# Optimization experiments

Hardware: AMD Instinct MI355X
Metric: run time of the kernel (lower is better)

## Reference

```python
import jax, jax.numpy as jnp
import numpy as np


def setup_inputs() -> dict:
    key = jax.random.key(0)
    k1, k2 = jax.random.split(key)
    B, T, D = 16, 2048, 1024
    inputs = jax.random.normal(k1, (B, T, D), dtype=jnp.float32)
    mask = jax.random.randint(k2, (B, T), 0, 2).astype(bool)
    return {"inputs": inputs, "mask": mask}


def reference(inputs, mask):
    """Batched stream compaction (JIT-compatible ragged representation).

    Original TF layer loops over the batch and, per sample, gathers the
    rows of inputs[i] where mask[i] is True, returning ragged lists of
    (collected_values, valid_indices). Since JAX requires static shapes,
    we return the padded-compacted equivalent:
      collected: [B, T, D]  valid rows moved to the front (order preserved),
                            invalid tail zeroed.
      valid_idx: [B, T]     original timestep index of each collected row,
                            -1 in the padded tail.
      counts:    [B]        number of valid rows per sample, i.e.
                            collected[i, :counts[i]] == ragged segment i.
    """
    # Stable argsort of the inverted mask puts valid positions first,
    # preserving their original order -> single-pass prefix-sum compaction.
    order = jnp.argsort(jnp.logical_not(mask), axis=1, stable=True)      # [B, T]
    sorted_valid = jnp.take_along_axis(mask, order, axis=1)              # [B, T]
    collected = jnp.take_along_axis(inputs, order[:, :, None], axis=1)   # [B, T, D]
    collected = jnp.where(sorted_valid[:, :, None], collected, 0.0)
    valid_idx = jnp.where(sorted_valid, order, -1)
    counts = jnp.sum(mask, axis=1)
    return collected, valid_idx, counts
```

## Files before the change

kernel.cpp:

```cpp
#include <hip/hip_runtime.h>


#define BB 16
#define TT 2048
#define DD 1024
#define ROW4 (DD / 4)

typedef float f4 __attribute__((ext_vector_type(4)));

__global__ __launch_bounds__(256) void scan_kernel(
    const int* __restrict__ mask,
    float* __restrict__ out_vidx,
    float* __restrict__ out_counts,
    int* __restrict__ ws_src,
    int* __restrict__ ws_cnt)
{
    const int b = blockIdx.x;
    const int tid = threadIdx.x;
    const int4* m4 = (const int4*)(mask + b * TT);

    int4 a0 = m4[tid * 2];
    int4 a1 = m4[tid * 2 + 1];
    int vals[8];
    vals[0] = (a0.x != 0); vals[1] = (a0.y != 0);
    vals[2] = (a0.z != 0); vals[3] = (a0.w != 0);
    vals[4] = (a1.x != 0); vals[5] = (a1.y != 0);
    vals[6] = (a1.z != 0); vals[7] = (a1.w != 0);
    int s = 0;
#pragma unroll
    for (int i = 0; i < 8; ++i) s += vals[i];

    __shared__ int sdata[256];
    sdata[tid] = s;
    __syncthreads();
#pragma unroll
    for (int off = 1; off < 256; off <<= 1) {
        int v = (tid >= off) ? sdata[tid - off] : 0;
        __syncthreads();
        sdata[tid] += v;
        __syncthreads();
    }
    const int excl = sdata[tid] - s;
    const int total = sdata[255];

    int pos = excl;
#pragma unroll
    for (int i = 0; i < 8; ++i) {
        if (vals[i]) {
            const int t = tid * 8 + i;
            ws_src[b * TT + pos] = t;
            out_vidx[b * TT + pos] = (float)t;
            ++pos;
        }
    }

    for (int c = total + tid; c < TT; c += 256) {
        out_vidx[b * TT + c] = -1.0f;
    }

    if (tid == 0) {
        ws_cnt[b] = total;
        out_counts[b] = (float)total;
    }
}

__global__ __launch_bounds__(256) void gather_kernel(
    const f4* __restrict__ in,
    const int* __restrict__ ws_src,
    const int* __restrict__ ws_cnt,
    f4* __restrict__ out)
{
    const int tid  = threadIdx.x;
    const int lrow = tid >> 5;
    const int lane = tid & 31;
    const int row  = blockIdx.x * 8 + lrow;
    const int b    = row >> 11;
    const int c    = row & (TT - 1);

    f4* dst = out + (size_t)row * ROW4;
    if (c < ws_cnt[b]) {
        const int src = ws_src[row];
        const f4* sp = in + ((size_t)(b << 11) + (size_t)src) * ROW4;
        f4 v[8];
#pragma unroll
        for (int j = 0; j < 8; ++j)
            v[j] = __builtin_nontemporal_load(sp + lane + j * 32);
#pragma unroll
        for (int j = 0; j < 8; ++j)
            __builtin_nontemporal_store(v[j], dst + lane + j * 32);
    } else {
        const f4 z = {0.f, 0.f, 0.f, 0.f};
#pragma unroll
        for (int j = 0; j < 8; ++j)
            __builtin_nontemporal_store(z, dst + lane + j * 32);
    }
}

extern "C" void kernel_launch(void* const* d_in, const int* in_sizes, int n_in,
                              void* d_out, int out_size, void* d_ws, size_t ws_size,
                              hipStream_t stream) {
    const float* inputs = (const float*)d_in[0];
    const int* mask = (const int*)d_in[1];

    float* out = (float*)d_out;
    float* out_collected = out;
    float* out_vidx = out + (size_t)BB * TT * DD;
    float* out_counts = out_vidx + (size_t)BB * TT;

    int* ws_src = (int*)d_ws;
    int* ws_cnt = ws_src + BB * TT;

    scan_kernel<<<BB, 256, 0, stream>>>(mask, out_vidx, out_counts, ws_src, ws_cnt);
    gather_kernel<<<BB * TT / 8, 256, 0, stream>>>(
        (const f4*)inputs, ws_src, ws_cnt, (f4*)out_collected);
}
```

Measured before the change: 218.8 us.

## Fuse mask scan into gather kernel with per-block redundant wave-shuffle scan

Merges the separate scan and gather kernels into one launch. Every gather block recomputes its batch's full 2048-element prefix scan, using wave shuffles plus a 4-entry shared-memory combine, and stores the compacted source indices in LDS. This removes the second launch, the serial dependency on a 16-block scan kernel, and the workspace round trip. The cost is 256x redundant mask reads and scans per batch, plus 8KB of LDS per block.

Measured after the change: 215.6 us (median of 2 runs). About the same (-1.4%).

```diff
diff --git a/kernel.cpp b/kernel.cpp
--- a/kernel.cpp
+++ b/kernel.cpp
@@ -8,17 +8,20 @@
 
 typedef float f4 __attribute__((ext_vector_type(4)));
 
-__global__ __launch_bounds__(256) void scan_kernel(
+__global__ __launch_bounds__(256) void fused_kernel(
     const int* __restrict__ mask,
+    const f4* __restrict__ in,
+    f4* __restrict__ out,
     float* __restrict__ out_vidx,
-    float* __restrict__ out_counts,
-    int* __restrict__ ws_src,
-    int* __restrict__ ws_cnt)
+    float* __restrict__ out_counts)
 {
-    const int b = blockIdx.x;
-    const int tid = threadIdx.x;
+    const int b    = blockIdx.x >> 8;
+    const int blk  = blockIdx.x & 255;
+    const int tid  = threadIdx.x;
+    const int lane = tid & 63;
+    const int wv   = tid >> 6;
+
     const int4* m4 = (const int4*)(mask + b * TT);
-
     int4 a0 = m4[tid * 2];
     int4 a1 = m4[tid * 2 + 1];
     int vals[8];
@@ -30,69 +33,55 @@
 #pragma unroll
     for (int i = 0; i < 8; ++i) s += vals[i];
 
-    __shared__ int sdata[256];
-    sdata[tid] = s;
+    int incl = s;
+#pragma unroll
+    for (int off = 1; off < 64; off <<= 1) {
+        int v = __shfl_up(incl, off, 64);
+        if (lane >= off) incl += v;
+    }
+
+    __shared__ int wsum[4];
+    __shared__ int ssrc[TT];
+    if (lane == 63) wsum[wv] = incl;
     __syncthreads();
+
+    int woff = 0;
 #pragma unroll
-    for (int off = 1; off < 256; off <<= 1) {
-        int v = (tid >= off) ? sdata[tid - off] : 0;
-        __syncthreads();
-        sdata[tid] += v;
-        __syncthreads();
-    }
-    const int excl = sdata[tid] - s;
-    const int total = sdata[255];
+    for (int w = 0; w < 4; ++w) woff += (w < wv) ? wsum[w] : 0;
+    const int cnt = wsum[0] + wsum[1] + wsum[2] + wsum[3];
 
-    int pos = excl;
+    int pos = woff + incl - s;
 #pragma unroll
     for (int i = 0; i < 8; ++i) {
-        if (vals[i]) {
-            const int t = tid * 8 + i;
-            ws_src[b * TT + pos] = t;
-            out_vidx[b * TT + pos] = (float)t;
-            ++pos;
-        }
+        if (vals[i]) ssrc[pos++] = tid * 8 + i;
+    }
+    __syncthreads();
+
+    if (blk == 0) {
+        for (int c = tid; c < TT; c += 256)
+            out_vidx[b * TT + c] = (c < cnt) ? (float)ssrc[c] : -1.0f;
+        if (tid == 0) out_counts[b] = (float)cnt;
     }
 
-    for (int c = total + tid; c < TT; c += 256) {
-        out_vidx[b * TT + c] = -1.0f;
-    }
-
-    if (tid == 0) {
-        ws_cnt[b] = total;
-        out_counts[b] = (float)total;
-    }
-}
-
-__global__ __launch_bounds__(256) void gather_kernel(
-    const f4* __restrict__ in,
-    const int* __restrict__ ws_src,
-    const int* __restrict__ ws_cnt,
-    f4* __restrict__ out)
-{
-    const int tid  = threadIdx.x;
     const int lrow = tid >> 5;
-    const int lane = tid & 31;
-    const int row  = blockIdx.x * 8 + lrow;
-    const int b    = row >> 11;
-    const int c    = row & (TT - 1);
-
-    f4* dst = out + (size_t)row * ROW4;
-    if (c < ws_cnt[b]) {
-        const int src = ws_src[row];
-        const f4* sp = in + ((size_t)(b << 11) + (size_t)src) * ROW4;
+    const int ln   = tid & 31;
+    const int c    = blk * 8 + lrow;
+    f4* dst = out + ((size_t)(b * TT + c)) * ROW4;
+    if (c < cnt) {
+        const int src = ssrc[c];
+        const f4* sp = in + ((size_t)(b * TT + src)) * ROW4;
         f4 v[8];
 #pragma unroll
         for (int j = 0; j < 8; ++j)
-            v[j] = __builtin_nontemporal_load(sp + lane + j * 32);
+            v[j] = __builtin_nontemporal_load(sp + ln + j * 32);
 #pragma unroll
         for (int j = 0; j < 8; ++j)
-            __builtin_nontemporal_store(v[j], dst + lane + j * 32);
+            __builtin_nontemporal_store(v[j], dst + ln + j * 32);
     } else {
         const f4 z = {0.f, 0.f, 0.f, 0.f};
 #pragma unroll
         for (int j = 0; j < 8; ++j)
-            __builtin_nontemporal_store(z, dst + lane + j * 32);
+            __builtin_nontemporal_store(z, dst + ln + j * 32);
     }
 }
 
@@ -107,10 +96,6 @@
     float* out_vidx = out + (size_t)BB * TT * DD;
     float* out_counts = out_vidx + (size_t)BB * TT;
 
-    int* ws_src = (int*)d_ws;
-    int* ws_cnt = ws_src + BB * TT;
-
-    scan_kernel<<<BB, 256, 0, stream>>>(mask, out_vidx, out_counts, ws_src, ws_cnt);
-    gather_kernel<<<BB * TT / 8, 256, 0, stream>>>(
-        (const f4*)inputs, ws_src, ws_cnt, (f4*)out_collected);
+    fused_kernel<<<BB * 256, 256, 0, stream>>>(
+        mask, (const f4*)inputs, (f4*)out_collected, out_vidx, out_counts);
 }
```
